# Optimization experiments

Hardware: AMD Instinct MI355X
Metric: run time of the kernel (lower is better)

Reference implementation:

```python
import jax, jax.numpy as jnp
import numpy as np

B, S, H, NH = 2, 2048, 1024, 16
HD = H // NH  # 64
EPS = 1e-5


def setup_inputs() -> dict:
    key = jax.random.key(0)
    ks = jax.random.split(key, 4)
    return {
        "hidden_states": jax.random.normal(ks[0], (B, S, H), dtype=jnp.float32),
        "W_attn": jax.random.normal(ks[1], (H, 3 * H), dtype=jnp.float32) * (1.0 / np.sqrt(H)),
        "b_attn": jnp.zeros((3 * H,), dtype=jnp.float32),
        "W_proj": jax.random.normal(ks[2], (H, H), dtype=jnp.float32) * (1.0 / np.sqrt(H)),
        "b_proj": jnp.zeros((H,), dtype=jnp.float32),
        "q_gamma": jnp.ones((HD,), dtype=jnp.float32),
        "q_beta": jnp.zeros((HD,), dtype=jnp.float32),
        "k_gamma": jnp.ones((HD,), dtype=jnp.float32),
        "k_beta": jnp.zeros((HD,), dtype=jnp.float32),
    }


def _layernorm(x, gamma, beta):
    mu = jnp.mean(x, axis=-1, keepdims=True)
    var = jnp.mean(jnp.square(x - mu), axis=-1, keepdims=True)
    return (x - mu) * jax.lax.rsqrt(var + EPS) * gamma + beta


def reference(hidden_states, W_attn, b_attn, W_proj, b_proj, q_gamma, q_beta, k_gamma, k_beta):
    b, s, h = hidden_states.shape
    qkv = hidden_states @ W_attn + b_attn  # [B,S,3H]
    q, k, v = jnp.split(qkv, 3, axis=-1)
    # [B,S,H] -> [B,NH,S,HD]
    def to_heads(t):
        return t.reshape(b, s, NH, HD).transpose(0, 2, 1, 3)
    q, k, v = to_heads(q), to_heads(k), to_heads(v)
    # QK LayerNorm over head_dim
    q = _layernorm(q, q_gamma, q_beta)
    k = _layernorm(k, k_gamma, k_beta)
    scale = HD ** (-0.5)
    scores = jnp.einsum("bhqd,bhkd->bhqk", q, k) * scale
    causal = jnp.tril(jnp.ones((s, s), dtype=bool))
    mask_value = jnp.finfo(scores.dtype).min
    scores = jnp.where(causal, scores, mask_value)
    attn = jax.nn.softmax(scores.astype(jnp.float32), axis=-1).astype(q.dtype)
    out = jnp.einsum("bhqk,bhkd->bhqd", attn, v)
    out = out.transpose(0, 2, 1, 3).reshape(b, s, h)
    out = out @ W_proj + b_proj
    return out
```

## Files before the change

kernel.cpp:

```cpp
#include <hip/hip_runtime.h>
#include <hip/hip_bf16.h>

typedef __bf16 bf16x8 __attribute__((ext_vector_type(8)));
typedef float f32x4 __attribute__((ext_vector_type(4)));

#define EPS 1e-5f
#define QSCALE 0.18033688011112042f

__device__ __forceinline__ unsigned short f2bf(float f) {
  union { float f; unsigned int i; } c; c.f = f;
  unsigned int r = c.i + 0x7FFFu + ((c.i >> 16) & 1u);
  return (unsigned short)(r >> 16);
}

__device__ __forceinline__ void transpose_tile(
    const float* __restrict__ in, unsigned short* __restrict__ out,
    int R, int C, int ct0, int rt0, unsigned short* S )
{
  const int t = threadIdx.x;
  const int r = t >> 2, c4 = (t & 3) * 16;
  {
    long base = (long)(rt0 + r) * C + ct0 + c4;
    float4 a = *(const float4*)&in[base];
    float4 b = *(const float4*)&in[base + 4];
    float4 c = *(const float4*)&in[base + 8];
    float4 d = *(const float4*)&in[base + 12];
    unsigned short v[16] = {f2bf(a.x), f2bf(a.y), f2bf(a.z), f2bf(a.w),
                            f2bf(b.x), f2bf(b.y), f2bf(b.z), f2bf(b.w),
                            f2bf(c.x), f2bf(c.y), f2bf(c.z), f2bf(c.w),
                            f2bf(d.x), f2bf(d.y), f2bf(d.z), f2bf(d.w)};
    *(uint4*)&S[r * 72 + c4]     = *(uint4*)&v[0];
    *(uint4*)&S[r * 72 + c4 + 8] = *(uint4*)&v[8];
  }
  __syncthreads();
  unsigned short tmp[16];
#pragma unroll
  for (int j = 0; j < 16; j++) tmp[j] = S[(c4 + j) * 72 + r];
  *(uint4*)&out[(long)(ct0 + r) * R + rt0 + c4]     = *(uint4*)&tmp[0];
  *(uint4*)&out[(long)(ct0 + r) * R + rt0 + c4 + 8] = *(uint4*)&tmp[8];
}

__global__ __launch_bounds__(256) void prep_kernel(
    const float* __restrict__ Wa, const float* __restrict__ Wp,
    const float* __restrict__ X,
    unsigned short* __restrict__ WaT, unsigned short* __restrict__ WpT,
    unsigned short* __restrict__ Xbf)
{
  __shared__ __align__(16) unsigned short S[64 * 72];
  const int id = blockIdx.x;
  if (id < 768) {
    transpose_tile(Wa, WaT, 1024, 3072, (id % 48) * 64, (id / 48) * 64, S);
  } else if (id < 1024) {
    const int i2 = id - 768;
    transpose_tile(Wp, WpT, 1024, 1024, (i2 % 16) * 64, (i2 / 16) * 64, S);
  } else {
    long i = ((long)(id - 1024) * 256 + threadIdx.x) * 16;
    float4 a = *(const float4*)&X[i];
    float4 b = *(const float4*)&X[i + 4];
    float4 c = *(const float4*)&X[i + 8];
    float4 d = *(const float4*)&X[i + 12];
    unsigned short v[16] = {f2bf(a.x), f2bf(a.y), f2bf(a.z), f2bf(a.w),
                            f2bf(b.x), f2bf(b.y), f2bf(b.z), f2bf(b.w),
                            f2bf(c.x), f2bf(c.y), f2bf(c.z), f2bf(c.w),
                            f2bf(d.x), f2bf(d.y), f2bf(d.z), f2bf(d.w)};
    *(uint4*)&Xbf[i]     = *(uint4*)&v[0];
    *(uint4*)&Xbf[i + 8] = *(uint4*)&v[8];
  }
}

__global__ __launch_bounds__(256) void qkv_ln_kernel(
    const float* __restrict__ Xf,
    const unsigned short* __restrict__ Xbf, int use_xbf,
    const unsigned short* __restrict__ WT,
    const float* __restrict__ bias,
    const float* __restrict__ qg, const float* __restrict__ qb,
    const float* __restrict__ kg, const float* __restrict__ kb,
    unsigned short* __restrict__ Qws, unsigned short* __restrict__ Kws)
{
  __shared__ __align__(16) unsigned short As[2][128 * 32];
  __shared__ __align__(16) unsigned short Bs[2][128 * 32];

  const int tid = threadIdx.x;
  const int w = tid >> 6, lane = tid & 63, quad = lane >> 4, l15 = lane & 15;
  const int mh = w & 1, nh = w >> 1;
  const int n0 = blockIdx.x * 128, m0 = blockIdx.y * 128;

  f32x4 acc[4][4];
#pragma unroll
  for (int i = 0; i < 4; i++)
#pragma unroll
    for (int j = 0; j < 4; j++) acc[i][j] = (f32x4){0.f, 0.f, 0.f, 0.f};

  const int sr2 = tid >> 1, sh2 = (tid & 1) * 16;

  if (use_xbf) {
    long xo = (long)(m0 + sr2) * 1024 + sh2;
    *(uint4*)&As[0][sr2 * 32 + sh2]     = *(const uint4*)&Xbf[xo];
    *(uint4*)&As[0][sr2 * 32 + sh2 + 8] = *(const uint4*)&Xbf[xo + 8];
  } else {
    long xo = (long)(m0 + sr2) * 1024 + sh2;
    float4 a0 = *(const float4*)&Xf[xo];
    float4 a1 = *(const float4*)&Xf[xo + 4];
    float4 a2 = *(const float4*)&Xf[xo + 8];
    float4 a3 = *(const float4*)&Xf[xo + 12];
    unsigned short v[16] = {f2bf(a0.x), f2bf(a0.y), f2bf(a0.z), f2bf(a0.w),
                            f2bf(a1.x), f2bf(a1.y), f2bf(a1.z), f2bf(a1.w),
                            f2bf(a2.x), f2bf(a2.y), f2bf(a2.z), f2bf(a2.w),
                            f2bf(a3.x), f2bf(a3.y), f2bf(a3.z), f2bf(a3.w)};
    *(uint4*)&As[0][sr2 * 32 + sh2]     = *(uint4*)&v[0];
    *(uint4*)&As[0][sr2 * 32 + sh2 + 8] = *(uint4*)&v[8];
  }
  {
    long wo = (long)(n0 + sr2) * 1024 + sh2;
    *(uint4*)&Bs[0][sr2 * 32 + sh2]     = *(const uint4*)&WT[wo];
    *(uint4*)&Bs[0][sr2 * 32 + sh2 + 8] = *(const uint4*)&WT[wo + 8];
  }
  __syncthreads();

  int buf = 0;
  for (int kt = 0; kt < 1024; kt += 32) {
    const int nbuf = buf ^ 1;
    const bool pf = (kt + 32) < 1024;
    uint4 xv0, xv1, wv0, wv1;
    float4 a0, a1, a2, a3;
    if (pf) {
      if (use_xbf) {
        long xo = (long)(m0 + sr2) * 1024 + kt + 32 + sh2;
        xv0 = *(const uint4*)&Xbf[xo];
        xv1 = *(const uint4*)&Xbf[xo + 8];
      } else {
        long xo = (long)(m0 + sr2) * 1024 + kt + 32 + sh2;
        a0 = *(const float4*)&Xf[xo];
        a1 = *(const float4*)&Xf[xo + 4];
        a2 = *(const float4*)&Xf[xo + 8];
        a3 = *(const float4*)&Xf[xo + 12];
      }
      long wo = (long)(n0 + sr2) * 1024 + kt + 32 + sh2;
      wv0 = *(const uint4*)&WT[wo];
      wv1 = *(const uint4*)&WT[wo + 8];
    }

    bf16x8 af[4], bfr[4];
#pragma unroll
    for (int mq = 0; mq < 4; mq++)
      af[mq] = *(const bf16x8*)&As[buf][(mh * 64 + mq * 16 + l15) * 32 + quad * 8];
#pragma unroll
    for (int nq = 0; nq < 4; nq++)
      bfr[nq] = *(const bf16x8*)&Bs[buf][(nh * 64 + nq * 16 + l15) * 32 + quad * 8];
#pragma unroll
    for (int mq = 0; mq < 4; mq++)
#pragma unroll
      for (int nq = 0; nq < 4; nq++)
        acc[mq][nq] = __builtin_amdgcn_mfma_f32_16x16x32_bf16(af[mq], bfr[nq], acc[mq][nq], 0, 0, 0);

    if (pf) {
      if (use_xbf) {
        *(uint4*)&As[nbuf][sr2 * 32 + sh2]     = xv0;
        *(uint4*)&As[nbuf][sr2 * 32 + sh2 + 8] = xv1;
      } else {
        unsigned short v[16] = {f2bf(a0.x), f2bf(a0.y), f2bf(a0.z), f2bf(a0.w),
                                f2bf(a1.x), f2bf(a1.y), f2bf(a1.z), f2bf(a1.w),
                                f2bf(a2.x), f2bf(a2.y), f2bf(a2.z), f2bf(a2.w),
                                f2bf(a3.x), f2bf(a3.y), f2bf(a3.z), f2bf(a3.w)};
        *(uint4*)&As[nbuf][sr2 * 32 + sh2]     = *(uint4*)&v[0];
        *(uint4*)&As[nbuf][sr2 * 32 + sh2 + 8] = *(uint4*)&v[8];
      }
      *(uint4*)&Bs[nbuf][sr2 * 32 + sh2]     = wv0;
      *(uint4*)&Bs[nbuf][sr2 * 32 + sh2 + 8] = wv1;
    }
    __syncthreads();
    buf = nbuf;
  }

#pragma unroll
  for (int nq = 0; nq < 4; nq++) {
    float bv = bias[n0 + nh * 64 + nq * 16 + l15];
#pragma unroll
    for (int mq = 0; mq < 4; mq++)
#pragma unroll
      for (int rr = 0; rr < 4; rr++) acc[mq][nq][rr] += bv;
  }

  const int g = (n0 >> 6) + nh;
  const bool isQ = g < 16;

  {
    float gv[4], bev[4];
#pragma unroll
    for (int nq = 0; nq < 4; nq++) {
      int d = nq * 16 + l15;
      gv[nq]  = isQ ? qg[d] : kg[d];
      bev[nq] = isQ ? qb[d] : kb[d];
      if (isQ) { gv[nq] *= QSCALE; bev[nq] *= QSCALE; }
    }
#pragma unroll
    for (int mq = 0; mq < 4; mq++)
#pragma unroll
      for (int rr = 0; rr < 4; rr++) {
        float s  = acc[mq][0][rr] + acc[mq][1][rr] + acc[mq][2][rr] + acc[mq][3][rr];
        float s2 = acc[mq][0][rr]*acc[mq][0][rr] + acc[mq][1][rr]*acc[mq][1][rr]
                 + acc[mq][2][rr]*acc[mq][2][rr] + acc[mq][3][rr]*acc[mq][3][rr];
#pragma unroll
        for (int off = 1; off < 16; off <<= 1) {
          s  += __shfl_xor(s,  off, 64);
          s2 += __shfl_xor(s2, off, 64);
        }
        float mu   = s * (1.0f / 64.0f);
        float var  = fmaxf(s2 * (1.0f / 64.0f) - mu * mu, 0.f);
        float rstd = rsqrtf(var + EPS);
#pragma unroll
        for (int nq = 0; nq < 4; nq++)
          acc[mq][nq][rr] = (acc[mq][nq][rr] - mu) * rstd * gv[nq] + bev[nq];
      }
  }

  unsigned short* dst = isQ ? Qws : Kws;
  const int head = isQ ? g : g - 16;

#pragma unroll
  for (int mq = 0; mq < 4; mq++)
#pragma unroll
    for (int rr = 0; rr < 4; rr++) {
      int m = m0 + mh * 64 + mq * 16 + quad * 4 + rr;
      int b = m >> 11, s = m & 2047;
      long base = ((long)((b * 16 + head) * 2048 + s)) * 64;
#pragma unroll
      for (int nq = 0; nq < 4; nq++)
        dst[base + nq * 16 + l15] = f2bf(acc[mq][nq][rr]);
    }
}

__global__ __launch_bounds__(256) void vt_kernel(
    const float* __restrict__ Xf,
    const unsigned short* __restrict__ Xbf, int use_xbf,
    const unsigned short* __restrict__ WvT,
    const float* __restrict__ bias,
    unsigned short* __restrict__ Vt)
{
  __shared__ __align__(16) unsigned short As[2][128 * 32];
  __shared__ __align__(16) unsigned short Bs[2][64 * 32];

  const int tid = threadIdx.x;
  const int w = tid >> 6, lane = tid & 63, quad = lane >> 4, l15 = lane & 15;
  const int mh = w & 1, nh = w >> 1;
  const int n0 = blockIdx.x * 64, m0 = blockIdx.y * 128, bz = blockIdx.z;
  const long xrow0 = (long)bz * 2048;

  f32x4 acc[4][2];
#pragma unroll
  for (int i = 0; i < 4; i++)
#pragma unroll
    for (int j = 0; j < 2; j++) acc[i][j] = (f32x4){0.f, 0.f, 0.f, 0.f};

  const int srA = tid >> 1, shA = (tid & 1) * 16;
  const int srB = tid >> 2, shB = (tid & 3) * 8;

  {
    long wo = (long)(m0 + srA) * 1024 + shA;
    *(uint4*)&As[0][srA * 32 + shA]     = *(const uint4*)&WvT[wo];
    *(uint4*)&As[0][srA * 32 + shA + 8] = *(const uint4*)&WvT[wo + 8];
  }
  if (use_xbf) {
    long xo = (xrow0 + n0 + srB) * 1024 + shB;
    *(uint4*)&Bs[0][srB * 32 + shB] = *(const uint4*)&Xbf[xo];
  } else {
    long xo = (xrow0 + n0 + srB) * 1024 + shB;
    float4 a0 = *(const float4*)&Xf[xo];
    float4 a1 = *(const float4*)&Xf[xo + 4];
    unsigned short v[8] = {f2bf(a0.x), f2bf(a0.y), f2bf(a0.z), f2bf(a0.w),
                           f2bf(a1.x), f2bf(a1.y), f2bf(a1.z), f2bf(a1.w)};
    *(uint4*)&Bs[0][srB * 32 + shB] = *(uint4*)v;
  }
  __syncthreads();

  int buf = 0;
  for (int kt = 0; kt < 1024; kt += 32) {
    const int nbuf = buf ^ 1;
    const bool pf = (kt + 32) < 1024;
    uint4 wv0, wv1, xv0;
    float4 a0, a1;
    if (pf) {
      long wo = (long)(m0 + srA) * 1024 + kt + 32 + shA;
      wv0 = *(const uint4*)&WvT[wo];
      wv1 = *(const uint4*)&WvT[wo + 8];
      long xo = (xrow0 + n0 + srB) * 1024 + kt + 32 + shB;
      if (use_xbf) {
        xv0 = *(const uint4*)&Xbf[xo];
      } else {
        a0 = *(const float4*)&Xf[xo];
        a1 = *(const float4*)&Xf[xo + 4];
      }
    }

    bf16x8 af[4], bfr[2];
#pragma unroll
    for (int mq = 0; mq < 4; mq++)
      af[mq] = *(const bf16x8*)&As[buf][(mh * 64 + mq * 16 + l15) * 32 + quad * 8];
#pragma unroll
    for (int nq = 0; nq < 2; nq++)
      bfr[nq] = *(const bf16x8*)&Bs[buf][(nh * 32 + nq * 16 + l15) * 32 + quad * 8];
#pragma unroll
    for (int mq = 0; mq < 4; mq++)
#pragma unroll
      for (int nq = 0; nq < 2; nq++)
        acc[mq][nq] = __builtin_amdgcn_mfma_f32_16x16x32_bf16(af[mq], bfr[nq], acc[mq][nq], 0, 0, 0);

    if (pf) {
      *(uint4*)&As[nbuf][srA * 32 + shA]     = wv0;
      *(uint4*)&As[nbuf][srA * 32 + shA + 8] = wv1;
      if (use_xbf) {
        *(uint4*)&Bs[nbuf][srB * 32 + shB] = xv0;
      } else {
        unsigned short v[8] = {f2bf(a0.x), f2bf(a0.y), f2bf(a0.z), f2bf(a0.w),
                               f2bf(a1.x), f2bf(a1.y), f2bf(a1.z), f2bf(a1.w)};
        *(uint4*)&Bs[nbuf][srB * 32 + shB] = *(uint4*)v;
      }
    }
    __syncthreads();
    buf = nbuf;
  }

  const long outb = (long)bz * 2097152;
#pragma unroll
  for (int mq = 0; mq < 4; mq++)
#pragma unroll
    for (int rr = 0; rr < 4; rr++) {
      int m = m0 + mh * 64 + mq * 16 + quad * 4 + rr;
      float bv = bias[2048 + m];
#pragma unroll
      for (int nq = 0; nq < 2; nq++) {
        int n = n0 + nh * 32 + nq * 16 + l15;
        Vt[outb + (long)m * 2048 + n] = f2bf(acc[mq][nq][rr] + bv);
      }
    }
}

__global__ __launch_bounds__(256) void attn_kernel(
    unsigned short* __restrict__ Qws,
    const unsigned short* __restrict__ Kws,
    const unsigned short* __restrict__ Vt)
{
  __shared__ __align__(16) unsigned short Ks[64 * 72];
  __shared__ __align__(16) unsigned short VTs[64 * 72];
  __shared__ __align__(16) unsigned short Ps[64 * 64];

  const int tid = threadIdx.x;
  const int w = tid >> 6, lane = tid & 63, quad = lane >> 4, l15 = lane & 15;
  const int bh = blockIdx.y;
  const long bhoff = (long)bh * 2048 * 64;
  const long bhv   = (long)bh * 131072;

  const int sr = tid >> 2, sc = (tid & 3) * 16;
  const int qsw = ((sr >> 2) & 3) << 4;
  const int sw = ((l15 >> 2) & 3) << 4;
  const int pc0 = (quad * 8) ^ sw;
  const int pc1 = (32 + quad * 8) ^ sw;

  bf16x8 ones;
  {
    union { unsigned short u[8]; bf16x8 v; } c;
#pragma unroll
    for (int i = 0; i < 8; i++) c.u[i] = 0x3F80u;
    ones = c.v;
  }

#pragma unroll
  for (int ph = 0; ph < 2; ph++) {
    const int qt = ph ? (31 - blockIdx.x) : blockIdx.x;
    const int qbase = qt * 64;
    const int jmax = qt + 1;

    if (ph) __syncthreads();

    *(uint4*)&Ps[sr * 64 + (sc ^ qsw)]       = *(const uint4*)&Qws[bhoff + (qbase + sr) * 64 + sc];
    *(uint4*)&Ps[sr * 64 + ((sc ^ qsw) + 8)] = *(const uint4*)&Qws[bhoff + (qbase + sr) * 64 + sc + 8];
    *(uint4*)&Ks[sr * 72 + sc]      = *(const uint4*)&Kws[bhoff + sr * 64 + sc];
    *(uint4*)&Ks[sr * 72 + sc + 8]  = *(const uint4*)&Kws[bhoff + sr * 64 + sc + 8];
    *(uint4*)&VTs[sr * 72 + sc]     = *(const uint4*)&Vt[bhv + sr * 2048 + sc];
    *(uint4*)&VTs[sr * 72 + sc + 8] = *(const uint4*)&Vt[bhv + sr * 2048 + sc + 8];
    __syncthreads();

    const bf16x8 qf0 = *(const bf16x8*)&Ps[(w * 16 + l15) * 64 + pc0];
    const bf16x8 qf1 = *(const bf16x8*)&Ps[(w * 16 + l15) * 64 + pc1];

    f32x4 o[4], osum;
#pragma unroll
    for (int i = 0; i < 4; i++) o[i] = (f32x4){0.f, 0.f, 0.f, 0.f};
    osum = (f32x4){0.f, 0.f, 0.f, 0.f};

    for (int j = 0; j < jmax; j++) {
      const int kb = j * 64;
      const bool pf = (j + 1) < jmax;
      uint4 pk0, pk1, pv0, pv1;
      if (pf) {
        const int kb1 = kb + 64;
        pk0 = *(const uint4*)&Kws[bhoff + (kb1 + sr) * 64 + sc];
        pk1 = *(const uint4*)&Kws[bhoff + (kb1 + sr) * 64 + sc + 8];
        pv0 = *(const uint4*)&Vt[bhv + sr * 2048 + kb1 + sc];
        pv1 = *(const uint4*)&Vt[bhv + sr * 2048 + kb1 + sc + 8];
      }

      f32x4 sacc[4];
#pragma unroll
      for (int i = 0; i < 4; i++) sacc[i] = (f32x4){0.f, 0.f, 0.f, 0.f};
#pragma unroll
      for (int nt = 0; nt < 4; nt++) {
        bf16x8 kf0 = *(const bf16x8*)&Ks[(nt * 16 + l15) * 72 + quad * 8];
        bf16x8 kf1 = *(const bf16x8*)&Ks[(nt * 16 + l15) * 72 + 32 + quad * 8];
        sacc[nt] = __builtin_amdgcn_mfma_f32_16x16x32_bf16(qf0, kf0, sacc[nt], 0, 0, 0);
        sacc[nt] = __builtin_amdgcn_mfma_f32_16x16x32_bf16(qf1, kf1, sacc[nt], 0, 0, 0);
      }

      const bool domask = (j == qt);
#pragma unroll
      for (int nt = 0; nt < 4; nt++)
#pragma unroll
        for (int rr = 0; rr < 4; rr++) {
          float p = exp2f(sacc[nt][rr]);
          if (domask) {
            int kcol = kb + nt * 16 + l15;
            int qrow = qbase + w * 16 + quad * 4 + rr;
            if (kcol > qrow) p = 0.f;
          }
          sacc[nt][rr] = p;
        }

#pragma unroll
      for (int rr = 0; rr < 4; rr++)
#pragma unroll
        for (int nt = 0; nt < 4; nt++)
          Ps[(w * 16 + quad * 4 + rr) * 64 + (((nt ^ quad) & 3) * 16 + l15)]
              = f2bf(sacc[nt][rr]);

      bf16x8 pfr0 = *(const bf16x8*)&Ps[(w * 16 + l15) * 64 + pc0];
      bf16x8 pfr1 = *(const bf16x8*)&Ps[(w * 16 + l15) * 64 + pc1];

      osum = __builtin_amdgcn_mfma_f32_16x16x32_bf16(pfr0, ones, osum, 0, 0, 0);
      osum = __builtin_amdgcn_mfma_f32_16x16x32_bf16(pfr1, ones, osum, 0, 0, 0);
#pragma unroll
      for (int dt = 0; dt < 4; dt++) {
        bf16x8 vf0 = *(const bf16x8*)&VTs[(dt * 16 + l15) * 72 + quad * 8];
        bf16x8 vf1 = *(const bf16x8*)&VTs[(dt * 16 + l15) * 72 + 32 + quad * 8];
        o[dt] = __builtin_amdgcn_mfma_f32_16x16x32_bf16(pfr0, vf0, o[dt], 0, 0, 0);
        o[dt] = __builtin_amdgcn_mfma_f32_16x16x32_bf16(pfr1, vf1, o[dt], 0, 0, 0);
      }

      if (pf) {
        __syncthreads();
        *(uint4*)&Ks[sr * 72 + sc]      = pk0;
        *(uint4*)&Ks[sr * 72 + sc + 8]  = pk1;
        *(uint4*)&VTs[sr * 72 + sc]     = pv0;
        *(uint4*)&VTs[sr * 72 + sc + 8] = pv1;
        __syncthreads();
      }
    }

#pragma unroll
    for (int rr = 0; rr < 4; rr++) {
      float inv = 1.0f / osum[rr];
      int row = qbase + w * 16 + quad * 4 + rr;
      long base = bhoff + (long)row * 64;
#pragma unroll
      for (int dt = 0; dt < 4; dt++)
        Qws[base + dt * 16 + l15] = f2bf(o[dt][rr] * inv);
    }
  }
}

__global__ __launch_bounds__(256) void proj_kernel(
    const unsigned short* __restrict__ AQ,
    const unsigned short* __restrict__ WT,
    const float* __restrict__ bias,
    float* __restrict__ Out)
{
  __shared__ __align__(16) unsigned short As[2][128 * 32];
  __shared__ __align__(16) unsigned short Bs[2][64 * 32];

  const int tid = threadIdx.x;
  const int w = tid >> 6, lane = tid & 63, quad = lane >> 4, l15 = lane & 15;
  const int mh = w & 1, nh = w >> 1;
  const int n0 = blockIdx.x * 64, m0 = blockIdx.y * 128;

  f32x4 acc[4][2];
#pragma unroll
  for (int i = 0; i < 4; i++)
#pragma unroll
    for (int j = 0; j < 2; j++) acc[i][j] = (f32x4){0.f, 0.f, 0.f, 0.f};

  const int srA = tid >> 1, shA = (tid & 1) * 16;
  const int srB = tid >> 2, shB = (tid & 3) * 8;
  const int m = m0 + srA, b = m >> 11, s = m & 2047;

  {
    const int h = shA >> 6, d = shA & 63;
    long ao = ((long)((b * 16 + h) * 2048 + s)) * 64 + d;
    *(uint4*)&As[0][srA * 32 + shA]     = *(const uint4*)&AQ[ao];
    *(uint4*)&As[0][srA * 32 + shA + 8] = *(const uint4*)&AQ[ao + 8];
    long wo = (long)(n0 + srB) * 1024 + shB;
    *(uint4*)&Bs[0][srB * 32 + shB] = *(const uint4*)&WT[wo];
  }
  __syncthreads();

  int buf = 0;
  for (int kt = 0; kt < 1024; kt += 32) {
    const int nbuf = buf ^ 1;
    const bool pf = (kt + 32) < 1024;
    uint4 av0, av1, wv0;
    if (pf) {
      const int k = kt + 32 + shA, h = k >> 6, d = k & 63;
      long ao = ((long)((b * 16 + h) * 2048 + s)) * 64 + d;
      av0 = *(const uint4*)&AQ[ao];
      av1 = *(const uint4*)&AQ[ao + 8];
      long wo = (long)(n0 + srB) * 1024 + kt + 32 + shB;
      wv0 = *(const uint4*)&WT[wo];
    }

    bf16x8 af[4], bfr[2];
#pragma unroll
    for (int mq = 0; mq < 4; mq++)
      af[mq] = *(const bf16x8*)&As[buf][(mh * 64 + mq * 16 + l15) * 32 + quad * 8];
#pragma unroll
    for (int nq = 0; nq < 2; nq++)
      bfr[nq] = *(const bf16x8*)&Bs[buf][(nh * 32 + nq * 16 + l15) * 32 + quad * 8];
#pragma unroll
    for (int mq = 0; mq < 4; mq++)
#pragma unroll
      for (int nq = 0; nq < 2; nq++)
        acc[mq][nq] = __builtin_amdgcn_mfma_f32_16x16x32_bf16(af[mq], bfr[nq], acc[mq][nq], 0, 0, 0);

    if (pf) {
      *(uint4*)&As[nbuf][srA * 32 + shA]     = av0;
      *(uint4*)&As[nbuf][srA * 32 + shA + 8] = av1;
      *(uint4*)&Bs[nbuf][srB * 32 + shB]     = wv0;
    }
    __syncthreads();
    buf = nbuf;
  }

#pragma unroll
  for (int nq = 0; nq < 2; nq++) {
    int n = n0 + nh * 32 + nq * 16 + l15;
    float bv = bias[n];
#pragma unroll
    for (int mq = 0; mq < 4; mq++)
#pragma unroll
      for (int rr = 0; rr < 4; rr++) {
        int mm = m0 + mh * 64 + mq * 16 + quad * 4 + rr;
        Out[(long)mm * 1024 + n] = acc[mq][nq][rr] + bv;
      }
  }
}

extern "C" void kernel_launch(void* const* d_in, const int* in_sizes, int n_in,
                              void* d_out, int out_size, void* d_ws, size_t ws_size,
                              hipStream_t stream) {
  const float* X  = (const float*)d_in[0];
  const float* Wa = (const float*)d_in[1];
  const float* ba = (const float*)d_in[2];
  const float* Wp = (const float*)d_in[3];
  const float* bp = (const float*)d_in[4];
  const float* qg = (const float*)d_in[5];
  const float* qb = (const float*)d_in[6];
  const float* kg = (const float*)d_in[7];
  const float* kb = (const float*)d_in[8];

  const long per = 2L * 16 * 2048 * 64;
  unsigned short* ws  = (unsigned short*)d_ws;
  unsigned short* Qws = ws;
  unsigned short* Kws = Qws + per;
  unsigned short* Vt  = Kws + per;

  const bool big = ws_size >= (size_t)(5L * per * 2);
  unsigned short *Xbf, *WaT, *WpT;
  if (big) {
    Xbf = Vt + per;
    WaT = Xbf + per;
    WpT = WaT + 3072L * 1024;
  } else {
    Xbf = Qws;
    WaT = Vt + per;
    WpT = WaT + 3072L * 1024;
  }
  unsigned short* WvT = WaT + 2048L * 1024;

  prep_kernel<<<big ? 2048 : 1024, 256, 0, stream>>>(Wa, Wp, X, WaT, WpT, Xbf);
  qkv_ln_kernel<<<dim3(16, 32), 256, 0, stream>>>(X, Xbf, big ? 1 : 0, WaT, ba,
                                                  qg, qb, kg, kb, Qws, Kws);
  vt_kernel<<<dim3(32, 8, 2), 256, 0, stream>>>(X, Xbf, big ? 1 : 0, WvT, ba, Vt);
  attn_kernel<<<dim3(16, 32), 256, 0, stream>>>(Qws, Kws, Vt);
  proj_kernel<<<dim3(16, 32), 256, 0, stream>>>(Qws, WpT, bp, (float*)d_out);
}
```

Measured before the change: 208.8 us.

## Merge QK and V projection kernels into one launch, remap attention blocks

Fuses the Q/K LayerNorm GEMM and the transposed-V GEMM into a single kernel that dispatches on block index, which removes one launch and lets the two GEMMs fill the GPU together. The attention grid becomes 1D, with block ids mapped so that neighbouring blocks work on different batch-heads, which may improve spread across XCDs and cache locality. The P-to-bf16 conversion in attention switches from round-to-nearest to truncation, which is cheaper but slightly less accurate. The fused kernel uses the larger shared-memory footprint for the V branch, which may lower occupancy there.

```diff
diff --git a/kernel.cpp b/kernel.cpp
--- a/kernel.cpp
+++ b/kernel.cpp
@@ -11,6 +11,10 @@
   union { float f; unsigned int i; } c; c.f = f;
   unsigned int r = c.i + 0x7FFFu + ((c.i >> 16) & 1u);
   return (unsigned short)(r >> 16);
+}
+__device__ __forceinline__ unsigned short f2bf_t(float f) {
+  union { float f; unsigned int i; } c; c.f = f;
+  return (unsigned short)(c.i >> 16);
 }
 
 __device__ __forceinline__ void transpose_tile(
@@ -68,14 +72,15 @@
   }
 }
 
-__global__ __launch_bounds__(256) void qkv_ln_kernel(
+__global__ __launch_bounds__(256) void qkvt_kernel(
     const float* __restrict__ Xf,
     const unsigned short* __restrict__ Xbf, int use_xbf,
     const unsigned short* __restrict__ WT,
     const float* __restrict__ bias,
     const float* __restrict__ qg, const float* __restrict__ qb,
     const float* __restrict__ kg, const float* __restrict__ kb,
-    unsigned short* __restrict__ Qws, unsigned short* __restrict__ Kws)
+    unsigned short* __restrict__ Qws, unsigned short* __restrict__ Kws,
+    unsigned short* __restrict__ Vt)
 {
   __shared__ __align__(16) unsigned short As[2][128 * 32];
   __shared__ __align__(16) unsigned short Bs[2][128 * 32];
@@ -83,256 +88,246 @@
   const int tid = threadIdx.x;
   const int w = tid >> 6, lane = tid & 63, quad = lane >> 4, l15 = lane & 15;
   const int mh = w & 1, nh = w >> 1;
-  const int n0 = blockIdx.x * 128, m0 = blockIdx.y * 128;
-
-  f32x4 acc[4][4];
-#pragma unroll
-  for (int i = 0; i < 4; i++)
-#pragma unroll
-    for (int j = 0; j < 4; j++) acc[i][j] = (f32x4){0.f, 0.f, 0.f, 0.f};
-
-  const int sr2 = tid >> 1, sh2 = (tid & 1) * 16;
-
-  if (use_xbf) {
-    long xo = (long)(m0 + sr2) * 1024 + sh2;
-    *(uint4*)&As[0][sr2 * 32 + sh2]     = *(const uint4*)&Xbf[xo];
-    *(uint4*)&As[0][sr2 * 32 + sh2 + 8] = *(const uint4*)&Xbf[xo + 8];
+  const int id = blockIdx.x;
+
+  if (id < 512) {
+    const int n0 = (id & 15) * 128, m0 = (id >> 4) * 128;
+
+    f32x4 acc[4][4];
+#pragma unroll
+    for (int i = 0; i < 4; i++)
+#pragma unroll
+      for (int j = 0; j < 4; j++) acc[i][j] = (f32x4){0.f, 0.f, 0.f, 0.f};
+
+    const int sr2 = tid >> 1, sh2 = (tid & 1) * 16;
+
+    if (use_xbf) {
+      long xo = (long)(m0 + sr2) * 1024 + sh2;
+      *(uint4*)&As[0][sr2 * 32 + sh2]     = *(const uint4*)&Xbf[xo];
+      *(uint4*)&As[0][sr2 * 32 + sh2 + 8] = *(const uint4*)&Xbf[xo + 8];
+    } else {
+      long xo = (long)(m0 + sr2) * 1024 + sh2;
+      float4 a0 = *(const float4*)&Xf[xo];
+      float4 a1 = *(const float4*)&Xf[xo + 4];
+      float4 a2 = *(const float4*)&Xf[xo + 8];
+      float4 a3 = *(const float4*)&Xf[xo + 12];
+      unsigned short v[16] = {f2bf(a0.x), f2bf(a0.y), f2bf(a0.z), f2bf(a0.w),
+                              f2bf(a1.x), f2bf(a1.y), f2bf(a1.z), f2bf(a1.w),
+                              f2bf(a2.x), f2bf(a2.y), f2bf(a2.z), f2bf(a2.w),
+                              f2bf(a3.x), f2bf(a3.y), f2bf(a3.z), f2bf(a3.w)};
+      *(uint4*)&As[0][sr2 * 32 + sh2]     = *(uint4*)&v[0];
+      *(uint4*)&As[0][sr2 * 32 + sh2 + 8] = *(uint4*)&v[8];
+    }
+    {
+      long wo = (long)(n0 + sr2) * 1024 + sh2;
+      *(uint4*)&Bs[0][sr2 * 32 + sh2]     = *(const uint4*)&WT[wo];
+      *(uint4*)&Bs[0][sr2 * 32 + sh2 + 8] = *(const uint4*)&WT[wo + 8];
+    }
+    __syncthreads();
+
+    int buf = 0;
+    for (int kt = 0; kt < 1024; kt += 32) {
+      const int nbuf = buf ^ 1;
+      const bool pf = (kt + 32) < 1024;
+      uint4 xv0, xv1, wv0, wv1;
+      float4 a0, a1, a2, a3;
+      if (pf) {
+        if (use_xbf) {
+          long xo = (long)(m0 + sr2) * 1024 + kt + 32 + sh2;
+          xv0 = *(const uint4*)&Xbf[xo];
+          xv1 = *(const uint4*)&Xbf[xo + 8];
+        } else {
+          long xo = (long)(m0 + sr2) * 1024 + kt + 32 + sh2;
+          a0 = *(const float4*)&Xf[xo];
+          a1 = *(const float4*)&Xf[xo + 4];
+          a2 = *(const float4*)&Xf[xo + 8];
+          a3 = *(const float4*)&Xf[xo + 12];
+        }
+        long wo = (long)(n0 + sr2) * 1024 + kt + 32 + sh2;
+        wv0 = *(const uint4*)&WT[wo];
+        wv1 = *(const uint4*)&WT[wo + 8];
+      }
+
+      bf16x8 af[4], bfr[4];
+#pragma unroll
+      for (int mq = 0; mq < 4; mq++)
+        af[mq] = *(const bf16x8*)&As[buf][(mh * 64 + mq * 16 + l15) * 32 + quad * 8];
+#pragma unroll
+      for (int nq = 0; nq < 4; nq++)
+        bfr[nq] = *(const bf16x8*)&Bs[buf][(nh * 64 + nq * 16 + l15) * 32 + quad * 8];
+#pragma unroll
+      for (int mq = 0; mq < 4; mq++)
+#pragma unroll
+        for (int nq = 0; nq < 4; nq++)
+          acc[mq][nq] = __builtin_amdgcn_mfma_f32_16x16x32_bf16(af[mq], bfr[nq], acc[mq][nq], 0, 0, 0);
+
+      if (pf) {
+        if (use_xbf) {
+          *(uint4*)&As[nbuf][sr2 * 32 + sh2]     = xv0;
+          *(uint4*)&As[nbuf][sr2 * 32 + sh2 + 8] = xv1;
+        } else {
+          unsigned short v[16] = {f2bf(a0.x), f2bf(a0.y), f2bf(a0.z), f2bf(a0.w),
+                                  f2bf(a1.x), f2bf(a1.y), f2bf(a1.z), f2bf(a1.w),
+                                  f2bf(a2.x), f2bf(a2.y), f2bf(a2.z), f2bf(a2.w),
+                                  f2bf(a3.x), f2bf(a3.y), f2bf(a3.z), f2bf(a3.w)};
+          *(uint4*)&As[nbuf][sr2 * 32 + sh2]     = *(uint4*)&v[0];
+          *(uint4*)&As[nbuf][sr2 * 32 + sh2 + 8] = *(uint4*)&v[8];
+        }
+        *(uint4*)&Bs[nbuf][sr2 * 32 + sh2]     = wv0;
+        *(uint4*)&Bs[nbuf][sr2 * 32 + sh2 + 8] = wv1;
+      }
+      __syncthreads();
+      buf = nbuf;
+    }
+
+#pragma unroll
+    for (int nq = 0; nq < 4; nq++) {
+      float bv = bias[n0 + nh * 64 + nq * 16 + l15];
+#pragma unroll
+      for (int mq = 0; mq < 4; mq++)
+#pragma unroll
+        for (int rr = 0; rr < 4; rr++) acc[mq][nq][rr] += bv;
+    }
+
+    const int g = (n0 >> 6) + nh;
+    const bool isQ = g < 16;
+    {
+      float gv[4], bev[4];
+#pragma unroll
+      for (int nq = 0; nq < 4; nq++) {
+        int d = nq * 16 + l15;
+        gv[nq]  = isQ ? qg[d] : kg[d];
+        bev[nq] = isQ ? qb[d] : kb[d];
+        if (isQ) { gv[nq] *= QSCALE; bev[nq] *= QSCALE; }
+      }
+#pragma unroll
+      for (int mq = 0; mq < 4; mq++)
+#pragma unroll
+        for (int rr = 0; rr < 4; rr++) {
+          float s  = acc[mq][0][rr] + acc[mq][1][rr] + acc[mq][2][rr] + acc[mq][3][rr];
+          float s2 = acc[mq][0][rr]*acc[mq][0][rr] + acc[mq][1][rr]*acc[mq][1][rr]
+                   + acc[mq][2][rr]*acc[mq][2][rr] + acc[mq][3][rr]*acc[mq][3][rr];
+#pragma unroll
+          for (int off = 1; off < 16; off <<= 1) {
+            s  += __shfl_xor(s,  off, 64);
+            s2 += __shfl_xor(s2, off, 64);
+          }
+          float mu   = s * (1.0f / 64.0f);
+          float var  = fmaxf(s2 * (1.0f / 64.0f) - mu * mu, 0.f);
+          float rstd = rsqrtf(var + EPS);
+#pragma unroll
+          for (int nq = 0; nq < 4; nq++)
+            acc[mq][nq][rr] = (acc[mq][nq][rr] - mu) * rstd * gv[nq] + bev[nq];
+        }
+    }
+
+    unsigned short* dst = isQ ? Qws : Kws;
+    const int head = isQ ? g : g - 16;
+#pragma unroll
+    for (int mq = 0; mq < 4; mq++)
+#pragma unroll
+      for (int rr = 0; rr < 4; rr++) {
+        int m = m0 + mh * 64 + mq * 16 + quad * 4 + rr;
+        int b = m >> 11, s = m & 2047;
+        long base = ((long)((b * 16 + head) * 2048 + s)) * 64;
+#pragma unroll
+        for (int nq = 0; nq < 4; nq++)
+          dst[base + nq * 16 + l15] = f2bf(acc[mq][nq][rr]);
+      }
   } else {
-    long xo = (long)(m0 + sr2) * 1024 + sh2;
-    float4 a0 = *(const float4*)&Xf[xo];
-    float4 a1 = *(const float4*)&Xf[xo + 4];
-    float4 a2 = *(const float4*)&Xf[xo + 8];
-    float4 a3 = *(const float4*)&Xf[xo + 12];
-    unsigned short v[16] = {f2bf(a0.x), f2bf(a0.y), f2bf(a0.z), f2bf(a0.w),
-                            f2bf(a1.x), f2bf(a1.y), f2bf(a1.z), f2bf(a1.w),
-                            f2bf(a2.x), f2bf(a2.y), f2bf(a2.z), f2bf(a2.w),
-                            f2bf(a3.x), f2bf(a3.y), f2bf(a3.z), f2bf(a3.w)};
-    *(uint4*)&As[0][sr2 * 32 + sh2]     = *(uint4*)&v[0];
-    *(uint4*)&As[0][sr2 * 32 + sh2 + 8] = *(uint4*)&v[8];
-  }
-  {
-    long wo = (long)(n0 + sr2) * 1024 + sh2;
-    *(uint4*)&Bs[0][sr2 * 32 + sh2]     = *(const uint4*)&WT[wo];
-    *(uint4*)&Bs[0][sr2 * 32 + sh2 + 8] = *(const uint4*)&WT[wo + 8];
-  }
-  __syncthreads();
-
-  int buf = 0;
-  for (int kt = 0; kt < 1024; kt += 32) {
-    const int nbuf = buf ^ 1;
-    const bool pf = (kt + 32) < 1024;
-    uint4 xv0, xv1, wv0, wv1;
-    float4 a0, a1, a2, a3;
-    if (pf) {
-      if (use_xbf) {
-        long xo = (long)(m0 + sr2) * 1024 + kt + 32 + sh2;
-        xv0 = *(const uint4*)&Xbf[xo];
-        xv1 = *(const uint4*)&Xbf[xo + 8];
-      } else {
-        long xo = (long)(m0 + sr2) * 1024 + kt + 32 + sh2;
-        a0 = *(const float4*)&Xf[xo];
-        a1 = *(const float4*)&Xf[xo + 4];
-        a2 = *(const float4*)&Xf[xo + 8];
-        a3 = *(const float4*)&Xf[xo + 12];
-      }
-      long wo = (long)(n0 + sr2) * 1024 + kt + 32 + sh2;
-      wv0 = *(const uint4*)&WT[wo];
-      wv1 = *(const uint4*)&WT[wo + 8];
-    }
-
-    bf16x8 af[4], bfr[4];
+    const int id2 = id - 512;
+    const int n0 = (id2 & 31) * 64, m0 = ((id2 >> 5) & 7) * 128, bz = id2 >> 8;
+    const long xrow0 = (long)bz * 2048;
+    const unsigned short* WvT = WT + 2048L * 1024;
+
+    f32x4 acc[4][2];
+#pragma unroll
+    for (int i = 0; i < 4; i++)
+#pragma unroll
+      for (int j = 0; j < 2; j++) acc[i][j] = (f32x4){0.f, 0.f, 0.f, 0.f};
+
+    const int srA = tid >> 1, shA = (tid & 1) * 16;
+    const int srB = tid >> 2, shB = (tid & 3) * 8;
+
+    {
+      long wo = (long)(m0 + srA) * 1024 + shA;
+      *(uint4*)&As[0][srA * 32 + shA]     = *(const uint4*)&WvT[wo];
+      *(uint4*)&As[0][srA * 32 + shA + 8] = *(const uint4*)&WvT[wo + 8];
+    }
+    if (use_xbf) {
+      long xo = (xrow0 + n0 + srB) * 1024 + shB;
+      *(uint4*)&Bs[0][srB * 32 + shB] = *(const uint4*)&Xbf[xo];
+    } else {
+      long xo = (xrow0 + n0 + srB) * 1024 + shB;
+      float4 a0 = *(const float4*)&Xf[xo];
+      float4 a1 = *(const float4*)&Xf[xo + 4];
+      unsigned short v[8] = {f2bf(a0.x), f2bf(a0.y), f2bf(a0.z), f2bf(a0.w),
+                             f2bf(a1.x), f2bf(a1.y), f2bf(a1.z), f2bf(a1.w)};
+      *(uint4*)&Bs[0][srB * 32 + shB] = *(uint4*)v;
+    }
+    __syncthreads();
+
+    int buf = 0;
+    for (int kt = 0; kt < 1024; kt += 32) {
+      const int nbuf = buf ^ 1;
+      const bool pf = (kt + 32) < 1024;
+      uint4 wv0, wv1, xv0;
+      float4 a0, a1;
+      if (pf) {
+        long wo = (long)(m0 + srA) * 1024 + kt + 32 + shA;
+        wv0 = *(const uint4*)&WvT[wo];
+        wv1 = *(const uint4*)&WvT[wo + 8];
+        long xo = (xrow0 + n0 + srB) * 1024 + kt + 32 + shB;
+        if (use_xbf) {
+          xv0 = *(const uint4*)&Xbf[xo];
+        } else {
+          a0 = *(const float4*)&Xf[xo];
+          a1 = *(const float4*)&Xf[xo + 4];
+        }
+      }
+
+      bf16x8 af[4], bfr[2];
+#pragma unroll
+      for (int mq = 0; mq < 4; mq++)
+        af[mq] = *(const bf16x8*)&As[buf][(mh * 64 + mq * 16 + l15) * 32 + quad * 8];
+#pragma unroll
+      for (int nq = 0; nq < 2; nq++)
+        bfr[nq] = *(const bf16x8*)&Bs[buf][(nh * 32 + nq * 16 + l15) * 32 + quad * 8];
+#pragma unroll
+      for (int mq = 0; mq < 4; mq++)
+#pragma unroll
+        for (int nq = 0; nq < 2; nq++)
+          acc[mq][nq] = __builtin_amdgcn_mfma_f32_16x16x32_bf16(af[mq], bfr[nq], acc[mq][nq], 0, 0, 0);
+
+      if (pf) {
+        *(uint4*)&As[nbuf][srA * 32 + shA]     = wv0;
+        *(uint4*)&As[nbuf][srA * 32 + shA + 8] = wv1;
+        if (use_xbf) {
+          *(uint4*)&Bs[nbuf][srB * 32 + shB] = xv0;
+        } else {
+          unsigned short v[8] = {f2bf(a0.x), f2bf(a0.y), f2bf(a0.z), f2bf(a0.w),
+                                 f2bf(a1.x), f2bf(a1.y), f2bf(a1.z), f2bf(a1.w)};
+          *(uint4*)&Bs[nbuf][srB * 32 + shB] = *(uint4*)v;
+        }
+      }
+      __syncthreads();
+      buf = nbuf;
+    }
+
+    const long outb = (long)bz * 2097152;
 #pragma unroll
     for (int mq = 0; mq < 4; mq++)
-      af[mq] = *(const bf16x8*)&As[buf][(mh * 64 + mq * 16 + l15) * 32 + quad * 8];
-#pragma unroll
-    for (int nq = 0; nq < 4; nq++)
-      bfr[nq] = *(const bf16x8*)&Bs[buf][(nh * 64 + nq * 16 + l15) * 32 + quad * 8];
-#pragma unroll
-    for (int mq = 0; mq < 4; mq++)
-#pragma unroll
-      for (int nq = 0; nq < 4; nq++)
-        acc[mq][nq] = __builtin_amdgcn_mfma_f32_16x16x32_bf16(af[mq], bfr[nq], acc[mq][nq], 0, 0, 0);
-
-    if (pf) {
-      if (use_xbf) {
-        *(uint4*)&As[nbuf][sr2 * 32 + sh2]     = xv0;
-        *(uint4*)&As[nbuf][sr2 * 32 + sh2 + 8] = xv1;
-      } else {
-        unsigned short v[16] = {f2bf(a0.x), f2bf(a0.y), f2bf(a0.z), f2bf(a0.w),
-                                f2bf(a1.x), f2bf(a1.y), f2bf(a1.z), f2bf(a1.w),
-                                f2bf(a2.x), f2bf(a2.y), f2bf(a2.z), f2bf(a2.w),
-                                f2bf(a3.x), f2bf(a3.y), f2bf(a3.z), f2bf(a3.w)};
-        *(uint4*)&As[nbuf][sr2 * 32 + sh2]     = *(uint4*)&v[0];
-        *(uint4*)&As[nbuf][sr2 * 32 + sh2 + 8] = *(uint4*)&v[8];
-      }
-      *(uint4*)&Bs[nbuf][sr2 * 32 + sh2]     = wv0;
-      *(uint4*)&Bs[nbuf][sr2 * 32 + sh2 + 8] = wv1;
-    }
-    __syncthreads();
-    buf = nbuf;
-  }
-
-#pragma unroll
-  for (int nq = 0; nq < 4; nq++) {
-    float bv = bias[n0 + nh * 64 + nq * 16 + l15];
-#pragma unroll
-    for (int mq = 0; mq < 4; mq++)
-#pragma unroll
-      for (int rr = 0; rr < 4; rr++) acc[mq][nq][rr] += bv;
-  }
-
-  const int g = (n0 >> 6) + nh;
-  const bool isQ = g < 16;
-
-  {
-    float gv[4], bev[4];
-#pragma unroll
-    for (int nq = 0; nq < 4; nq++) {
-      int d = nq * 16 + l15;
-      gv[nq]  = isQ ? qg[d] : kg[d];
-      bev[nq] = isQ ? qb[d] : kb[d];
-      if (isQ) { gv[nq] *= QSCALE; bev[nq] *= QSCALE; }
-    }
-#pragma unroll
-    for (int mq = 0; mq < 4; mq++)
 #pragma unroll
       for (int rr = 0; rr < 4; rr++) {
-        float s  = acc[mq][0][rr] + acc[mq][1][rr] + acc[mq][2][rr] + acc[mq][3][rr];
-        float s2 = acc[mq][0][rr]*acc[mq][0][rr] + acc[mq][1][rr]*acc[mq][1][rr]
-                 + acc[mq][2][rr]*acc[mq][2][rr] + acc[mq][3][rr]*acc[mq][3][rr];
-#pragma unroll
-        for (int off = 1; off < 16; off <<= 1) {
-          s  += __shfl_xor(s,  off, 64);
-          s2 += __shfl_xor(s2, off, 64);
-        }
-        float mu   = s * (1.0f / 64.0f);
-        float var  = fmaxf(s2 * (1.0f / 64.0f) - mu * mu, 0.f);
-        float rstd = rsqrtf(var + EPS);
-#pragma unroll
-        for (int nq = 0; nq < 4; nq++)
-          acc[mq][nq][rr] = (acc[mq][nq][rr] - mu) * rstd * gv[nq] + bev[nq];
-      }
-  }
-
-  unsigned short* dst = isQ ? Qws : Kws;
-  const int head = isQ ? g : g - 16;
-
-#pragma unroll
-  for (int mq = 0; mq < 4; mq++)
-#pragma unroll
-    for (int rr = 0; rr < 4; rr++) {
-      int m = m0 + mh * 64 + mq * 16 + quad * 4 + rr;
-      int b = m >> 11, s = m & 2047;
-      long base = ((long)((b * 16 + head) * 2048 + s)) * 64;
-#pragma unroll
-      for (int nq = 0; nq < 4; nq++)
-        dst[base + nq * 16 + l15] = f2bf(acc[mq][nq][rr]);
-    }
-}
-
-__global__ __launch_bounds__(256) void vt_kernel(
-    const float* __restrict__ Xf,
-    const unsigned short* __restrict__ Xbf, int use_xbf,
-    const unsigned short* __restrict__ WvT,
-    const float* __restrict__ bias,
-    unsigned short* __restrict__ Vt)
-{
-  __shared__ __align__(16) unsigned short As[2][128 * 32];
-  __shared__ __align__(16) unsigned short Bs[2][64 * 32];
-
-  const int tid = threadIdx.x;
-  const int w = tid >> 6, lane = tid & 63, quad = lane >> 4, l15 = lane & 15;
-  const int mh = w & 1, nh = w >> 1;
-  const int n0 = blockIdx.x * 64, m0 = blockIdx.y * 128, bz = blockIdx.z;
-  const long xrow0 = (long)bz * 2048;
-
-  f32x4 acc[4][2];
-#pragma unroll
-  for (int i = 0; i < 4; i++)
-#pragma unroll
-    for (int j = 0; j < 2; j++) acc[i][j] = (f32x4){0.f, 0.f, 0.f, 0.f};
-
-  const int srA = tid >> 1, shA = (tid & 1) * 16;
-  const int srB = tid >> 2, shB = (tid & 3) * 8;
-
-  {
-    long wo = (long)(m0 + srA) * 1024 + shA;
-    *(uint4*)&As[0][srA * 32 + shA]     = *(const uint4*)&WvT[wo];
-    *(uint4*)&As[0][srA * 32 + shA + 8] = *(const uint4*)&WvT[wo + 8];
-  }
-  if (use_xbf) {
-    long xo = (xrow0 + n0 + srB) * 1024 + shB;
-    *(uint4*)&Bs[0][srB * 32 + shB] = *(const uint4*)&Xbf[xo];
-  } else {
-    long xo = (xrow0 + n0 + srB) * 1024 + shB;
-    float4 a0 = *(const float4*)&Xf[xo];
-    float4 a1 = *(const float4*)&Xf[xo + 4];
-    unsigned short v[8] = {f2bf(a0.x), f2bf(a0.y), f2bf(a0.z), f2bf(a0.w),
-                           f2bf(a1.x), f2bf(a1.y), f2bf(a1.z), f2bf(a1.w)};
-    *(uint4*)&Bs[0][srB * 32 + shB] = *(uint4*)v;
-  }
-  __syncthreads();
-
-  int buf = 0;
-  for (int kt = 0; kt < 1024; kt += 32) {
-    const int nbuf = buf ^ 1;
-    const bool pf = (kt + 32) < 1024;
-    uint4 wv0, wv1, xv0;
-    float4 a0, a1;
-    if (pf) {
-      long wo = (long)(m0 + srA) * 1024 + kt + 32 + shA;
-      wv0 = *(const uint4*)&WvT[wo];
-      wv1 = *(const uint4*)&WvT[wo + 8];
-      long xo = (xrow0 + n0 + srB) * 1024 + kt + 32 + shB;
-      if (use_xbf) {
-        xv0 = *(const uint4*)&Xbf[xo];
-      } else {
-        a0 = *(const float4*)&Xf[xo];
-        a1 = *(const float4*)&Xf[xo + 4];
-      }
-    }
-
-    bf16x8 af[4], bfr[2];
-#pragma unroll
-    for (int mq = 0; mq < 4; mq++)
-      af[mq] = *(const bf16x8*)&As[buf][(mh * 64 + mq * 16 + l15) * 32 + quad * 8];
-#pragma unroll
-    for (int nq = 0; nq < 2; nq++)
-      bfr[nq] = *(const bf16x8*)&Bs[buf][(nh * 32 + nq * 16 + l15) * 32 + quad * 8];
-#pragma unroll
-    for (int mq = 0; mq < 4; mq++)
-#pragma unroll
-      for (int nq = 0; nq < 2; nq++)
-        acc[mq][nq] = __builtin_amdgcn_mfma_f32_16x16x32_bf16(af[mq], bfr[nq], acc[mq][nq], 0, 0, 0);
-
-    if (pf) {
-      *(uint4*)&As[nbuf][srA * 32 + shA]     = wv0;
-      *(uint4*)&As[nbuf][srA * 32 + shA + 8] = wv1;
-      if (use_xbf) {
-        *(uint4*)&Bs[nbuf][srB * 32 + shB] = xv0;
-      } else {
-        unsigned short v[8] = {f2bf(a0.x), f2bf(a0.y), f2bf(a0.z), f2bf(a0.w),
-                               f2bf(a1.x), f2bf(a1.y), f2bf(a1.z), f2bf(a1.w)};
-        *(uint4*)&Bs[nbuf][srB * 32 + shB] = *(uint4*)v;
-      }
-    }
-    __syncthreads();
-    buf = nbuf;
-  }
-
-  const long outb = (long)bz * 2097152;
-#pragma unroll
-  for (int mq = 0; mq < 4; mq++)
-#pragma unroll
-    for (int rr = 0; rr < 4; rr++) {
-      int m = m0 + mh * 64 + mq * 16 + quad * 4 + rr;
-      float bv = bias[2048 + m];
-#pragma unroll
-      for (int nq = 0; nq < 2; nq++) {
-        int n = n0 + nh * 32 + nq * 16 + l15;
-        Vt[outb + (long)m * 2048 + n] = f2bf(acc[mq][nq][rr] + bv);
-      }
-    }
+        int m = m0 + mh * 64 + mq * 16 + quad * 4 + rr;
+        float bv = bias[2048 + m];
+#pragma unroll
+        for (int nq = 0; nq < 2; nq++) {
+          int n = n0 + nh * 32 + nq * 16 + l15;
+          Vt[outb + (long)m * 2048 + n] = f2bf(acc[mq][nq][rr] + bv);
+        }
+      }
+  }
 }
 
 __global__ __launch_bounds__(256) void attn_kernel(
@@ -346,7 +341,9 @@
 
   const int tid = threadIdx.x;
   const int w = tid >> 6, lane = tid & 63, quad = lane >> 4, l15 = lane & 15;
-  const int bh = blockIdx.y;
+  const int id = blockIdx.x;
+  const int bh = (id & 7) * 4 + ((id >> 3) & 3);
+  const int x  = id >> 5;
   const long bhoff = (long)bh * 2048 * 64;
   const long bhv   = (long)bh * 131072;
 
@@ -366,7 +363,7 @@
 
 #pragma unroll
   for (int ph = 0; ph < 2; ph++) {
-    const int qt = ph ? (31 - blockIdx.x) : blockIdx.x;
+    const int qt = ph ? (31 - x) : x;
     const int qbase = qt * 64;
     const int jmax = qt + 1;
 
@@ -430,7 +427,7 @@
 #pragma unroll
         for (int nt = 0; nt < 4; nt++)
           Ps[(w * 16 + quad * 4 + rr) * 64 + (((nt ^ quad) & 3) * 16 + l15)]
-              = f2bf(sacc[nt][rr]);
+              = f2bf_t(sacc[nt][rr]);
 
       bf16x8 pfr0 = *(const bf16x8*)&Ps[(w * 16 + l15) * 64 + pc0];
       bf16x8 pfr1 = *(const bf16x8*)&Ps[(w * 16 + l15) * 64 + pc1];
@@ -581,12 +578,10 @@
     WaT = Vt + per;
     WpT = WaT + 3072L * 1024;
   }
-  unsigned short* WvT = WaT + 2048L * 1024;
 
   prep_kernel<<<big ? 2048 : 1024, 256, 0, stream>>>(Wa, Wp, X, WaT, WpT, Xbf);
-  qkv_ln_kernel<<<dim3(16, 32), 256, 0, stream>>>(X, Xbf, big ? 1 : 0, WaT, ba,
-                                                  qg, qb, kg, kb, Qws, Kws);
-  vt_kernel<<<dim3(32, 8, 2), 256, 0, stream>>>(X, Xbf, big ? 1 : 0, WvT, ba, Vt);
-  attn_kernel<<<dim3(16, 32), 256, 0, stream>>>(Qws, Kws, Vt);
+  qkvt_kernel<<<1024, 256, 0, stream>>>(X, Xbf, big ? 1 : 0, WaT, ba,
+                                        qg, qb, kg, kb, Qws, Kws, Vt);
+  attn_kernel<<<512, 256, 0, stream>>>(Qws, Kws, Vt);
   proj_kernel<<<dim3(16, 32), 256, 0, stream>>>(Qws, WpT, bp, (float*)d_out);
 }
```

Measured after the change: 208.3 us. About the same (-0.2%).
